# Kernel optimization log

Hardware: AMD Instinct MI355X
Metric: run time of the kernel (lower is better)

The kernel has to match this reference:

```python
import jax, jax.numpy as jnp
import numpy as np
import math

HS_MIN = 1e-07
MASK_BOUND = 5e-08


def setup_inputs() -> dict:
    key = jax.random.key(0)
    N, B, D = 256, 128, 784
    k0, k1, k2 = jax.random.split(key, 3)
    bandwidth = (4.0 * np.sqrt(math.pi) / (math.pi ** 4 * N)) ** 0.2
    return {
        "x": jax.random.normal(k0, (B, D), jnp.float32),
        "log_det": jnp.zeros((B,), jnp.float32),
        "datapoints": jax.random.normal(k1, (N, D), jnp.float32),
        "log_hs": jnp.full((N, D), np.log(bandwidth), jnp.float32),
        "kde_weights": jnp.zeros((N, D), jnp.float32),
        "vs": jax.random.normal(k2, (D, D), jnp.float32),
    }


def _householder(vs):
    # Q = prod_i (I - 2 v_i v_i^T), applied as rank-1 updates via scan.
    D = vs.shape[1]
    def step(Q, v):
        vn = v / jnp.linalg.norm(v)
        return Q - 2.0 * jnp.outer(Q @ vn, vn), None
    Q, _ = jax.lax.scan(step, jnp.eye(D, dtype=vs.dtype), vs)
    return Q


def _kde_logs(x, datapoints, log_hs, kde_weights):
    # Shared [N,B,D] diff/softplus term feeding log_cdf, log_sf, log_pdf.
    hs = jnp.maximum(jnp.exp(log_hs), HS_MIN)
    log_hs_c = jnp.maximum(log_hs, math.log(HS_MIN))
    u = -(x[None, ...] - datapoints[:, None, :]) / hs[:, None, :]  # [N,B,D]
    w = (kde_weights - jax.nn.logsumexp(kde_weights, axis=0, keepdims=True))[:, None, :]
    sp = jax.nn.softplus(u)
    log_cdf = jax.nn.logsumexp(-sp + w, axis=0)                          # [B,D]
    log_sf = jax.nn.logsumexp(u - sp + w, axis=0)                        # [B,D]
    log_pdf = jax.nn.logsumexp(u - log_hs_c[:, None, :] - 2.0 * sp + w, axis=0)
    return log_cdf, log_sf, log_pdf


def reference(x, log_det, datapoints, log_hs, kde_weights, vs):
    log_cdf_l, log_sf_l, log_pdf = _kde_logs(x, datapoints, log_hs, kde_weights)
    cdf_l = jnp.exp(log_cdf_l)

    cdf_mask = ((cdf_l > MASK_BOUND) & (cdf_l < 1.0 - MASK_BOUND)).astype(x.dtype)
    cdf_l_good = cdf_l * cdf_mask + 0.5 * (1.0 - cdf_mask)
    inverse_l = jax.scipy.special.ndtri(cdf_l_good)

    cdf_mask_right = (cdf_l >= 1.0 - MASK_BOUND).astype(x.dtype)
    cdf_l_bad_right_log = log_sf_l * cdf_mask_right + (-1.0) * (1.0 - cdf_mask_right)
    inverse_l = inverse_l + jnp.sqrt(-2.0 * cdf_l_bad_right_log) * cdf_mask_right

    cdf_mask_left = (cdf_l <= MASK_BOUND).astype(x.dtype)
    cdf_l_bad_left_log = log_cdf_l * cdf_mask_left + (-1.0) * (1.0 - cdf_mask_left)
    inverse_l = inverse_l - jnp.sqrt(-2.0 * cdf_l_bad_left_log) * cdf_mask_left

    log_norm = -0.5 * inverse_l ** 2 - 0.5 * math.log(2.0 * math.pi)
    log_gauss_deriv = (
        log_norm * cdf_mask
        + (jnp.log(jnp.sqrt(-2.0 * cdf_l_bad_left_log)) - log_cdf_l) * cdf_mask_left
        + (jnp.log(jnp.sqrt(-2.0 * cdf_l_bad_right_log)) - log_sf_l) * cdf_mask_right
    )
    log_det = log_det + jnp.sum(log_pdf - log_gauss_deriv, axis=-1)

    Q = _householder(vs)
    x_out = inverse_l @ Q
    return x_out, log_det
```

## Files before the change

### kernel.cpp

```cpp
#include <hip/hip_runtime.h>
#include <math.h>

#define NP 256
#define BB 128
#define DD 784
#define HS_MIN 1e-7f
#define LOG_HS_MIN -16.11809565095832f
#define LOG_MB -16.811242831518264f
#define NEG_HALF_LOG_2PI -0.9189385332046727f
#define W 8
#define NW 98

__device__ double ndtri_logs(float log_cdf_f, float log_sf_f) {
    double lp = (double)log_cdf_f;
    double ls = (double)log_sf_f;
    double p = (double)__expf(log_cdf_f);
    double q = p - 0.5;
    if (fabs(q) <= 0.425) {
        double r = 0.180625 - q * q;
        double num = (((((((2.5090809287301226727e3 * r + 3.3430575583588128105e4) * r
                         + 6.7265770927008700853e4) * r + 4.5921953931549871457e4) * r
                         + 1.3731693765509461125e4) * r + 1.9715909503065514427e3) * r
                         + 1.3314166789178437745e2) * r + 3.3871328727963666080e0);
        double den = (((((((5.2264952788528545610e3 * r + 2.8729085735721942674e4) * r
                         + 3.9307895800092710610e4) * r + 2.1213794301586595867e4) * r
                         + 5.3941960214247511077e3) * r + 6.8718700749205790830e2) * r
                         + 4.2313330701600911252e1) * r + 1.0);
        return q * num / den;
    }
    double r = (q < 0.0) ? sqrt(-lp) : sqrt(-ls);
    double v;
    if (r <= 5.0) {
        r -= 1.6;
        double num = (((((((7.74545014278341407640e-4 * r + 2.27238449892691845833e-2) * r
                         + 2.41780725177450611770e-1) * r + 1.27045825245236838258e0) * r
                         + 3.64784832476320460504e0) * r + 5.76949722146069140550e0) * r
                         + 4.63033784615654529590e0) * r + 1.42343711074968357734e0);
        double den = (((((((1.05075007164441684324e-9 * r + 5.47593808499534494600e-4) * r
                         + 1.51986665636164571966e-2) * r + 1.48103976427480074590e-1) * r
                         + 6.89767334985100004550e-1) * r + 1.67638483018380384940e0) * r
                         + 2.05319162663775882187e0) * r + 1.0);
        v = num / den;
    } else {
        r -= 5.0;
        double num = (((((((2.01033439929228813265e-7 * r + 2.71155556874348757815e-5) * r
                         + 1.24266094738807843860e-3) * r + 2.65321895265761230930e-2) * r
                         + 2.96560571828504891230e-1) * r + 1.78482653991729133580e0) * r
                         + 5.46378491116411436990e0) * r + 6.65790464350110377720e0);
        double den = (((((((2.04426310338993978564e-15 * r + 1.42151175831644588870e-7) * r
                         + 1.84631831751005468180e-5) * r + 7.86869131145613259100e-4) * r
                         + 1.48753612908506148525e-2) * r + 1.36929880922735805310e-1) * r
                         + 5.99832206555887937690e-1) * r + 1.0);
        v = num / den;
    }
    return (q < 0.0) ? -v : v;
}

__global__ __launch_bounds__(256) void k_kde(const float* __restrict__ kw,
                                             const float* __restrict__ log_hs,
                                             const float* __restrict__ dp,
                                             const float* __restrict__ x,
                                             float* __restrict__ Y,
                                             float* __restrict__ T) {
    __shared__ float red[4];
    __shared__ float4 pkL[NP];
    int d = blockIdx.x;
    int n = threadIdx.x;

    float a = kw[n * DD + d];
    float m = a;
    #pragma unroll
    for (int off = 32; off; off >>= 1) m = fmaxf(m, __shfl_xor(m, off, 64));
    if ((n & 63) == 0) red[n >> 6] = m;
    __syncthreads();
    m = fmaxf(fmaxf(red[0], red[1]), fmaxf(red[2], red[3]));
    __syncthreads();
    float e = __expf(a - m);
    #pragma unroll
    for (int off = 32; off; off >>= 1) e += __shfl_xor(e, off, 64);
    if ((n & 63) == 0) red[n >> 6] = e;
    __syncthreads();
    float lse = m + __logf(red[0] + red[1] + red[2] + red[3]);

    {
        int idx = n * DD + d;
        float lh = log_hs[idx];
        float hs = fmaxf(__expf(lh), HS_MIN);
        float lhc = fmaxf(lh, LOG_HS_MIN);
        float wv = a - lse;
        pkL[n] = make_float4(dp[idx], 1.f / hs, __expf(wv), __expf(wv - lhc));
    }
    __syncthreads();

    if (n < BB) {
        int b = n;
        float xv = x[b * DD + d];
        float s1 = 0.f, s2 = 0.f, s3 = 0.f;
        for (int k = 0; k < NP; ++k) {
            float4 c = pkL[k];
            float u = (c.x - xv) * c.y;
            float ee = __expf(-fabsf(u));
            float r = 1.f / (1.f + ee);
            float base = c.z * r;
            float eh = (u >= 0.f) ? ee : 1.f;
            float el = (u >= 0.f) ? 1.f : ee;
            s1 += base * eh;
            s2 += base * el;
            s3 += c.w * (ee * r * r);
        }
        float log_cdf = __logf(s1);
        float log_sf  = __logf(s2);
        float log_pdf = __logf(s3);

        bool right = (log_sf  <= LOG_MB);
        bool left  = (log_cdf <= LOG_MB);

        float inv, lgd;
        if (right) {
            float t2 = -2.f * log_sf;
            inv = sqrtf(t2);
            lgd = 0.5f * __logf(t2) - log_sf;
        } else if (left) {
            float t2 = -2.f * log_cdf;
            inv = -sqrtf(t2);
            lgd = 0.5f * __logf(t2) - log_cdf;
        } else {
            inv = (float)ndtri_logs(log_cdf, log_sf);
            lgd = -0.5f * inv * inv + NEG_HALF_LOG_2PI;
        }
        Y[b * DD + d] = inv;
        T[b * DD + d] = log_pdf - lgd;
    }
}

__global__ __launch_bounds__(256) void k_vngram(const float* __restrict__ vs,
                                                float* __restrict__ VN,
                                                float* __restrict__ G) {
    __shared__ float L[W * DD];
    __shared__ float red[4];
    __shared__ float nrm[W];
    int wi = blockIdx.x;
    int t = threadIdx.x;
    const float* src = vs + (size_t)wi * (W * DD);
    for (int j = t; j < W * DD; j += 256) L[j] = src[j];
    __syncthreads();

    for (int r = 0; r < W; ++r) {
        float ss = 0.f;
        for (int j = t; j < DD; j += 256) {
            float v = L[r * DD + j];
            ss += v * v;
        }
        #pragma unroll
        for (int off = 32; off; off >>= 1) ss += __shfl_down(ss, off, 64);
        if ((t & 63) == 0) red[t >> 6] = ss;
        __syncthreads();
        if (t == 0) nrm[r] = rsqrtf(red[0] + red[1] + red[2] + red[3]);
        __syncthreads();
    }

    for (int j = t; j < W * DD; j += 256) {
        int r = j / DD;
        float v = L[j] * nrm[r];
        L[j] = v;
        VN[(size_t)wi * (W * DD) + j] = v;
    }
    __syncthreads();

    if (t < 64) {
        int k = t >> 3, i = t & 7;
        const float4* a = (const float4*)(L + k * DD);
        const float4* b = (const float4*)(L + i * DD);
        float s = 0.f;
        for (int j = 0; j < DD / 4; ++j) {
            float4 av = a[j], bv = b[j];
            s += av.x * bv.x + av.y * bv.y + av.z * bv.z + av.w * bv.w;
        }
        G[wi * 64 + k * 8 + i] = s;
    }
}

__device__ __forceinline__ float wave_red_sum(float x) {
    x += __int_as_float(__builtin_amdgcn_update_dpp(0, __float_as_int(x), 0x111, 0xf, 0xf, true));
    x += __int_as_float(__builtin_amdgcn_update_dpp(0, __float_as_int(x), 0x112, 0xf, 0xf, true));
    x += __int_as_float(__builtin_amdgcn_update_dpp(0, __float_as_int(x), 0x114, 0xf, 0xf, true));
    x += __int_as_float(__builtin_amdgcn_update_dpp(0, __float_as_int(x), 0x118, 0xf, 0xf, true));
    x += __int_as_float(__builtin_amdgcn_update_dpp(0, __float_as_int(x), 0x142, 0xa, 0xf, true));
    x += __int_as_float(__builtin_amdgcn_update_dpp(0, __float_as_int(x), 0x143, 0xc, 0xf, true));
    return __int_as_float(__builtin_amdgcn_readlane(__float_as_int(x), 63));
}

__global__ __launch_bounds__(64, 1) void k_house(const float* __restrict__ Yin,
                                                 const float* __restrict__ T,
                                                 const float* __restrict__ ld_in,
                                                 const float* __restrict__ VN,
                                                 const float* __restrict__ G,
                                                 float* __restrict__ out) {
    __shared__ float gld[NW * 64];
    const int b = blockIdx.x;
    const int l = threadIdx.x;
    const int toff = 768 + (l & 15);
    const bool thas = (l < 16);

    {
        float s = 0.f;
        #pragma unroll
        for (int i = 0; i < 12; ++i) s += T[b * DD + 64 * i + l];
        if (thas) s += T[b * DD + 768 + l];
        float tot = wave_red_sum(s);
        if (l == 0) out[BB * DD + b] = ld_in[b] + tot;
    }

    for (int i = l; i < NW * 64; i += 64) gld[i] = G[i];
    __syncthreads();

    float4 y[3];
    float ytl;
    #pragma unroll
    for (int i = 0; i < 3; ++i)
        y[i] = *(const float4*)(Yin + b * DD + 256 * i + 4 * l);
    ytl = thas ? Yin[b * DD + toff] : 0.f;

    for (int wi = 0; wi < NW; ++wi) {
        const float* Vw = VN + (size_t)wi * (W * DD);
        const float* Gw = gld + wi * 64;

        float4 v[W][3];
        float vt[W];
        #pragma unroll
        for (int r = 0; r < W; ++r) {
            const float* vr = Vw + r * DD;
            #pragma unroll
            for (int i = 0; i < 3; ++i)
                v[r][i] = *(const float4*)(vr + 256 * i + 4 * l);
            vt[r] = thas ? vr[toff] : 0.f;
        }

        float p[W];
        #pragma unroll
        for (int r = 0; r < W; ++r) {
            float s = 0.f;
            #pragma unroll
            for (int i = 0; i < 3; ++i) {
                s += y[i].x * v[r][i].x + y[i].y * v[r][i].y
                   + y[i].z * v[r][i].z + y[i].w * v[r][i].w;
            }
            s += ytl * vt[r];
            p[r] = wave_red_sum(s);
        }

        float sv[W];
        #pragma unroll
        for (int r = 0; r < W; ++r) {
            float acc = p[r];
            #pragma unroll
            for (int k = 0; k < W; ++k)
                if (k < r) acc -= 2.f * Gw[k * 8 + r] * sv[k];
            sv[r] = acc;
        }

        #pragma unroll
        for (int r = 0; r < W; ++r) {
            float c = 2.f * sv[r];
            #pragma unroll
            for (int i = 0; i < 3; ++i) {
                y[i].x -= c * v[r][i].x;  y[i].y -= c * v[r][i].y;
                y[i].z -= c * v[r][i].z;  y[i].w -= c * v[r][i].w;
            }
            ytl -= c * vt[r];
        }
    }

    #pragma unroll
    for (int i = 0; i < 3; ++i)
        *(float4*)(out + b * DD + 256 * i + 4 * l) = y[i];
    if (thas)
        out[b * DD + toff] = ytl;
}

extern "C" void kernel_launch(void* const* d_in, const int* in_sizes, int n_in,
                              void* d_out, int out_size, void* d_ws, size_t ws_size,
                              hipStream_t stream) {
    const float* x      = (const float*)d_in[0];
    const float* ld_in  = (const float*)d_in[1];
    const float* dp     = (const float*)d_in[2];
    const float* log_hs = (const float*)d_in[3];
    const float* kw     = (const float*)d_in[4];
    const float* vs     = (const float*)d_in[5];
    float* out = (float*)d_out;

    float* ws   = (float*)d_ws;
    float* Y    = ws + 1024;
    float* T    = Y + BB * DD;
    float* VN   = T + BB * DD;
    float* G    = VN + DD * DD;

    k_vngram<<<NW, 256, 0, stream>>>(vs, VN, G);
    k_kde<<<DD, 256, 0, stream>>>(kw, log_hs, dp, x, Y, T);
    k_house<<<BB, 64, 0, stream>>>(Y, T, ld_in, VN, G, out);
}
```

Measured before the change: 235.3 us.

## Fuse vector-normalize/Gram kernel with KDE kernel and split N across all threads

Merges the Householder vector normalization/Gram kernel and the KDE kernel into one launch, with block index choosing the role, so the two independent stages run concurrently and one launch is removed. In the KDE part all 256 threads now work: each half of the block covers 128 datapoints for the same batch row and the partial sums are combined through shared memory, instead of leaving half the threads idle. The cost is that the shared buffer is sized for the Gram role (about 25KB), which can lower occupancy for KDE blocks, and there is an extra barrier.

```diff
diff --git a/kernel.cpp b/kernel.cpp
--- a/kernel.cpp
+++ b/kernel.cpp
@@ -56,16 +56,68 @@
     return (q < 0.0) ? -v : v;
 }
 
-__global__ __launch_bounds__(256) void k_kde(const float* __restrict__ kw,
-                                             const float* __restrict__ log_hs,
-                                             const float* __restrict__ dp,
-                                             const float* __restrict__ x,
-                                             float* __restrict__ Y,
-                                             float* __restrict__ T) {
-    __shared__ float red[4];
-    __shared__ float4 pkL[NP];
-    int d = blockIdx.x;
-    int n = threadIdx.x;
+__global__ __launch_bounds__(256) void k_fused(const float* __restrict__ vs,
+                                               float* __restrict__ VN,
+                                               float* __restrict__ G,
+                                               const float* __restrict__ kw,
+                                               const float* __restrict__ log_hs,
+                                               const float* __restrict__ dp,
+                                               const float* __restrict__ x,
+                                               float* __restrict__ Y,
+                                               float* __restrict__ T) {
+    __shared__ __align__(16) float smem[W * DD + 16];
+    int t = threadIdx.x;
+
+    if (blockIdx.x < NW) {
+        float* L   = smem;
+        float* red = smem + W * DD;
+        float* nrm = smem + W * DD + 4;
+        int wi = blockIdx.x;
+        const float* src = vs + (size_t)wi * (W * DD);
+        for (int j = t; j < W * DD; j += 256) L[j] = src[j];
+        __syncthreads();
+
+        for (int r = 0; r < W; ++r) {
+            float ss = 0.f;
+            for (int j = t; j < DD; j += 256) {
+                float v = L[r * DD + j];
+                ss += v * v;
+            }
+            #pragma unroll
+            for (int off = 32; off; off >>= 1) ss += __shfl_down(ss, off, 64);
+            if ((t & 63) == 0) red[t >> 6] = ss;
+            __syncthreads();
+            if (t == 0) nrm[r] = rsqrtf(red[0] + red[1] + red[2] + red[3]);
+            __syncthreads();
+        }
+
+        for (int j = t; j < W * DD; j += 256) {
+            int r = j / DD;
+            float v = L[j] * nrm[r];
+            L[j] = v;
+            VN[(size_t)wi * (W * DD) + j] = v;
+        }
+        __syncthreads();
+
+        if (t < 64) {
+            int k = t >> 3, i = t & 7;
+            const float4* a = (const float4*)(L + k * DD);
+            const float4* b = (const float4*)(L + i * DD);
+            float s = 0.f;
+            for (int j = 0; j < DD / 4; ++j) {
+                float4 av = a[j], bv = b[j];
+                s += av.x * bv.x + av.y * bv.y + av.z * bv.z + av.w * bv.w;
+            }
+            G[wi * 64 + k * 8 + i] = s;
+        }
+        return;
+    }
+
+    float*  red  = smem;
+    float4* pkL  = (float4*)(smem + 4);
+    float*  comb = smem + 4 + 4 * NP;
+    int d = blockIdx.x - NW;
+    int n = t;
 
     float a = kw[n * DD + d];
     float m = a;
@@ -92,22 +144,34 @@
     }
     __syncthreads();
 
-    if (n < BB) {
-        int b = n;
-        float xv = x[b * DD + d];
-        float s1 = 0.f, s2 = 0.f, s3 = 0.f;
-        for (int k = 0; k < NP; ++k) {
-            float4 c = pkL[k];
-            float u = (c.x - xv) * c.y;
-            float ee = __expf(-fabsf(u));
-            float r = 1.f / (1.f + ee);
-            float base = c.z * r;
-            float eh = (u >= 0.f) ? ee : 1.f;
-            float el = (u >= 0.f) ? 1.f : ee;
-            s1 += base * eh;
-            s2 += base * el;
-            s3 += c.w * (ee * r * r);
-        }
+    int b = n & 127;
+    int h = n >> 7;
+    float xv = x[b * DD + d];
+    float s1 = 0.f, s2 = 0.f, s3 = 0.f;
+    int k0 = h * 128;
+    #pragma unroll 4
+    for (int k = k0; k < k0 + 128; ++k) {
+        float4 c = pkL[k];
+        float u = (c.x - xv) * c.y;
+        float ee = __expf(-fabsf(u));
+        float r = 1.f / (1.f + ee);
+        float base = c.z * r;
+        float eh = (u >= 0.f) ? ee : 1.f;
+        float el = (u >= 0.f) ? 1.f : ee;
+        s1 += base * eh;
+        s2 += base * el;
+        s3 += c.w * (ee * r * r);
+    }
+    if (h == 1) {
+        comb[b * 3 + 0] = s1;
+        comb[b * 3 + 1] = s2;
+        comb[b * 3 + 2] = s3;
+    }
+    __syncthreads();
+    if (h == 0) {
+        s1 += comb[b * 3 + 0];
+        s2 += comb[b * 3 + 1];
+        s3 += comb[b * 3 + 2];
         float log_cdf = __logf(s1);
         float log_sf  = __logf(s2);
         float log_pdf = __logf(s3);
@@ -133,53 +197,6 @@
     }
 }
 
-__global__ __launch_bounds__(256) void k_vngram(const float* __restrict__ vs,
-                                                float* __restrict__ VN,
-                                                float* __restrict__ G) {
-    __shared__ float L[W * DD];
-    __shared__ float red[4];
-    __shared__ float nrm[W];
-    int wi = blockIdx.x;
-    int t = threadIdx.x;
-    const float* src = vs + (size_t)wi * (W * DD);
-    for (int j = t; j < W * DD; j += 256) L[j] = src[j];
-    __syncthreads();
-
-    for (int r = 0; r < W; ++r) {
-        float ss = 0.f;
-        for (int j = t; j < DD; j += 256) {
-            float v = L[r * DD + j];
-            ss += v * v;
-        }
-        #pragma unroll
-        for (int off = 32; off; off >>= 1) ss += __shfl_down(ss, off, 64);
-        if ((t & 63) == 0) red[t >> 6] = ss;
-        __syncthreads();
-        if (t == 0) nrm[r] = rsqrtf(red[0] + red[1] + red[2] + red[3]);
-        __syncthreads();
-    }
-
-    for (int j = t; j < W * DD; j += 256) {
-        int r = j / DD;
-        float v = L[j] * nrm[r];
-        L[j] = v;
-        VN[(size_t)wi * (W * DD) + j] = v;
-    }
-    __syncthreads();
-
-    if (t < 64) {
-        int k = t >> 3, i = t & 7;
-        const float4* a = (const float4*)(L + k * DD);
-        const float4* b = (const float4*)(L + i * DD);
-        float s = 0.f;
-        for (int j = 0; j < DD / 4; ++j) {
-            float4 av = a[j], bv = b[j];
-            s += av.x * bv.x + av.y * bv.y + av.z * bv.z + av.w * bv.w;
-        }
-        G[wi * 64 + k * 8 + i] = s;
-    }
-}
-
 __device__ __forceinline__ float wave_red_sum(float x) {
     x += __int_as_float(__builtin_amdgcn_update_dpp(0, __float_as_int(x), 0x111, 0xf, 0xf, true));
     x += __int_as_float(__builtin_amdgcn_update_dpp(0, __float_as_int(x), 0x112, 0xf, 0xf, true));
@@ -295,7 +312,6 @@
     float* VN   = T + BB * DD;
     float* G    = VN + DD * DD;
 
-    k_vngram<<<NW, 256, 0, stream>>>(vs, VN, G);
-    k_kde<<<DD, 256, 0, stream>>>(kw, log_hs, dp, x, Y, T);
+    k_fused<<<NW + DD, 256, 0, stream>>>(vs, VN, G, kw, log_hs, dp, x, Y, T);
     k_house<<<BB, 64, 0, stream>>>(Y, T, ld_in, VN, G, out);
 }
```

Result: faster. 223.2 us (-5.1%).
